# Kernel tuning notes

Hardware: AMD Instinct MI355X
Metric: run time of the kernel (lower is better)

The kernel has to match this reference:

```python
import jax, jax.numpy as jnp
import numpy as np
import math

B, T = 64, 2000
RNN_DIM, EMB_DIM, ATT_DIM = 1024, 512, 128
STATIC_CH, STATIC_K = 8, 21
DYN_CH, DYN_K = 8, 21
PRIOR_LEN, ALPHA, BETA = 11, 0.1, 0.9


def _betabinom_pmf(k, n, a, b):
    lg = math.lgamma
    return math.exp(lg(n + 1) - lg(k + 1) - lg(n - k + 1)
                    + lg(k + a) + lg(n - k + b) - lg(n + a + b)
                    - (lg(a) + lg(b) - lg(a + b)))


def setup_inputs() -> dict:
    key = jax.random.key(0)
    ks = jax.random.split(key, 12)
    query = jax.random.normal(ks[0], (B, RNN_DIM), jnp.float32)
    memory = jax.random.normal(ks[1], (B, T, EMB_DIM), jnp.float32)
    a = jax.random.uniform(ks[2], (B, T), jnp.float32)
    alignment_pre = a / jnp.sum(a, axis=1, keepdims=True)  # valid attention distribution
    mask = jnp.zeros((B, T), dtype=bool)
    s = 1.0 / math.sqrt(RNN_DIM)
    W_w = jax.random.uniform(ks[3], (ATT_DIM, RNN_DIM), jnp.float32, -s, s)
    W_b = jax.random.uniform(ks[4], (ATT_DIM,), jnp.float32, -s, s)
    V_w = jax.random.normal(ks[5], (DYN_CH * DYN_K, ATT_DIM), jnp.float32) * 0.05
    F_w = jax.random.normal(ks[6], (STATIC_CH, 1, STATIC_K), jnp.float32) * 0.1
    U_w = jax.random.normal(ks[7], (ATT_DIM, STATIC_CH), jnp.float32) * 0.1
    T_w = jax.random.normal(ks[8], (ATT_DIM, DYN_CH), jnp.float32) * 0.1
    T_b = jax.random.normal(ks[9], (ATT_DIM,), jnp.float32) * 0.05
    v_w = jax.random.normal(ks[10], (1, ATT_DIM), jnp.float32) * 0.1
    P_np = np.array([_betabinom_pmf(k, PRIOR_LEN - 1, ALPHA, BETA) for k in range(PRIOR_LEN)], np.float32)
    P = jnp.asarray(P_np[::-1].copy())  # buffer: flipped beta-binomial prior
    return {"attention_hidden_state": query, "memory": memory, "alignment_pre": alignment_pre,
            "mask": mask, "W_w": W_w, "W_b": W_b, "V_w": V_w, "F_w": F_w,
            "U_w": U_w, "T_w": T_w, "T_b": T_b, "v_w": v_w, "P": P}


def _conv1d(lhs, rhs, pad, groups=1):
    # lhs [N,C,T], rhs [O,C//groups,K]; cross-correlation, matching torch conv1d
    return jax.lax.conv_general_dilated(lhs, rhs, (1,), [pad],
                                        dimension_numbers=("NCH", "OIH", "NCH"),
                                        feature_group_count=groups)


def reference(attention_hidden_state, memory, alignment_pre, mask,
              W_w, W_b, V_w, F_w, U_w, T_w, T_b, v_w, P):
    b, t = alignment_pre.shape
    # log of causal beta-binomial prior: left-pad by prior_length-1, valid conv
    p = _conv1d(alignment_pre[:, None, :], P.reshape(1, 1, -1), (PRIOR_LEN - 1, 0))[:, 0, :]
    p = jnp.log(jnp.clip(p, 1e-6))
    # per-sample dynamic kernels: [B, dyn_ch*K]
    G = jnp.tanh(attention_hidden_state @ W_w.T + W_b) @ V_w.T
    g = _conv1d(alignment_pre[None, :, :], G.reshape(b * DYN_CH, 1, DYN_K),
                ((DYN_K - 1) // 2, (DYN_K - 1) // 2), groups=b)  # [1, B*dyn_ch, T]
    g = g.reshape(b, DYN_CH, t).transpose(0, 2, 1)  # [B, T, dyn_ch]
    # static conv features
    f = _conv1d(alignment_pre[:, None, :], F_w,
                ((STATIC_K - 1) // 2, (STATIC_K - 1) // 2)).transpose(0, 2, 1)  # [B, T, static_ch]
    e = (jnp.tanh(f @ U_w.T + g @ T_w.T + T_b) @ v_w.T)[..., 0] + p  # [B, T]
    e = jnp.where(mask, -jnp.inf, e)
    attention_weights = jax.nn.softmax(e, axis=1)
    attention_context = jnp.einsum("bt,bte->be", attention_weights, memory)
    return attention_context, attention_weights
```

## Files before the change

### kernel.cpp

```cpp
#include <hip/hip_runtime.h>

#define B_   64
#define T_   2000
#define RNN_ 1024
#define EMB_ 512
#define ATT_ 128
#define CH_  8
#define K_   21
#define PL_  11
#define GSZ  168
#define ECHK 128
#define NEC  16
#define CCHK 40
#define NCC  50

typedef float vf4 __attribute__((ext_vector_type(4)));

__device__ __forceinline__ float fast_tanh(float x) {
    float ax = fabsf(x);
    float e  = __expf(2.0f * ax);
    float t  = 1.0f - 2.0f / (e + 1.0f);
    return copysignf(t, x);
}

__global__ __launch_bounds__(256) void k_gen_dyn(
    const float* __restrict__ q, const float* __restrict__ Ww,
    const float* __restrict__ Wb, const float* __restrict__ Vw,
    float* __restrict__ G, float* __restrict__ out_ctx)
{
    __shared__ float sq[RNN_];
    __shared__ float part[256];
    __shared__ float sh[ATT_];
    const int b = blockIdx.x, tid = threadIdx.x;
    for (int i = tid; i < EMB_; i += 256) out_ctx[b * EMB_ + i] = 0.f;
    for (int i = tid; i < RNN_; i += 256) sq[i] = q[b * RNN_ + i];
    __syncthreads();
    {
        const int row = tid & 127, half = tid >> 7;
        const float4* wr = reinterpret_cast<const float4*>(Ww + row * RNN_ + half * (RNN_ / 2));
        const float4* qr = reinterpret_cast<const float4*>(sq + half * (RNN_ / 2));
        float acc = 0.f;
        #pragma unroll 8
        for (int i = 0; i < RNN_ / 8; ++i) {
            float4 w4 = wr[i], q4 = qr[i];
            acc += w4.x * q4.x + w4.y * q4.y + w4.z * q4.z + w4.w * q4.w;
        }
        part[tid] = acc;
    }
    __syncthreads();
    if (tid < ATT_) sh[tid] = fast_tanh(part[tid] + part[tid + 128] + Wb[tid]);
    __syncthreads();
    for (int o = tid; o < GSZ; o += 256) {
        const float4* vr = reinterpret_cast<const float4*>(Vw + o * ATT_);
        const float4* hr = reinterpret_cast<const float4*>(sh);
        float acc = 0.f;
        #pragma unroll 8
        for (int i = 0; i < ATT_ / 4; ++i) {
            float4 v4 = vr[i], h4 = hr[i];
            acc += v4.x * h4.x + v4.y * h4.y + v4.z * h4.z + v4.w * h4.w;
        }
        G[b * GSZ + o] = acc;
    }
}

__global__ __launch_bounds__(256) void k_energy(
    const float* __restrict__ a,  const float* __restrict__ G,
    const float* __restrict__ Fw, const float* __restrict__ Uw,
    const float* __restrict__ Tw, const float* __restrict__ Tb,
    const float* __restrict__ vw, const float* __restrict__ P,
    const unsigned char* __restrict__ mask,
    float* __restrict__ pws, float* __restrict__ sred)
{
    __shared__ float sA[ECHK + K_ - 1];
    __shared__ float sFG[K_ * 16];
    __shared__ float sUT[ATT_ * 16];
    __shared__ float sTb[ATT_], sV[ATT_], sPr[PL_];
    __shared__ float sQ[2 * ECHK];
    __shared__ float red[4];
    const int b = blockIdx.x, chunk = blockIdx.y, tid = threadIdx.x;
    const int t0 = chunk * ECHK;
    const int tloc = tid & (ECHK - 1);
    const int h = tid >> 7;

    for (int j = tid; j < ECHK + K_ - 1; j += 256) {
        int idx = t0 - 10 + j;
        sA[j] = (idx >= 0 && idx < T_) ? a[b * T_ + idx] : 0.f;
    }
    for (int j = tid; j < 2 * GSZ; j += 256) {
        if (j < GSZ) sFG[(j % K_) * 16 + (j / K_)] = Fw[j];
        else { int jj = j - GSZ; sFG[(jj % K_) * 16 + 8 + (jj / K_)] = G[b * GSZ + jj]; }
    }
    for (int j = tid; j < ATT_ * CH_; j += 256) {
        int d = j >> 3, c = j & 7;
        sUT[d * 16 + c]     = Uw[j];
        sUT[d * 16 + 8 + c] = Tw[j];
    }
    if (tid < ATT_) { sTb[tid] = Tb[tid]; sV[tid] = vw[tid]; }
    if (tid < PL_)  sPr[tid] = P[tid];
    __syncthreads();

    float fg[16];
    #pragma unroll
    for (int i = 0; i < 16; ++i) fg[i] = 0.f;
    #pragma unroll
    for (int k = 0; k < K_; ++k) {
        float av = sA[tloc + k];
        const float4* fp = reinterpret_cast<const float4*>(&sFG[k * 16]);
        float4 x0 = fp[0], x1 = fp[1], x2 = fp[2], x3 = fp[3];
        fg[0]  += x0.x * av; fg[1]  += x0.y * av; fg[2]  += x0.z * av; fg[3]  += x0.w * av;
        fg[4]  += x1.x * av; fg[5]  += x1.y * av; fg[6]  += x1.z * av; fg[7]  += x1.w * av;
        fg[8]  += x2.x * av; fg[9]  += x2.y * av; fg[10] += x2.z * av; fg[11] += x2.w * av;
        fg[12] += x3.x * av; fg[13] += x3.y * av; fg[14] += x3.z * av; fg[15] += x3.w * av;
    }

    float accQ = 0.f;
    const int d0 = h * 64;
    #pragma unroll 4
    for (int dd = 0; dd < 64; ++dd) {
        const int d = d0 + dd;
        const float4* up = reinterpret_cast<const float4*>(&sUT[d * 16]);
        float4 u0 = up[0], u1 = up[1], u2 = up[2], u3 = up[3];
        float s0 = u0.x * fg[0]  + u0.y * fg[1]  + u0.z * fg[2]  + u0.w * fg[3];
        float s1 = u1.x * fg[4]  + u1.y * fg[5]  + u1.z * fg[6]  + u1.w * fg[7];
        float s2 = u2.x * fg[8]  + u2.y * fg[9]  + u2.z * fg[10] + u2.w * fg[11];
        float s3 = u3.x * fg[12] + u3.y * fg[13] + u3.z * fg[14] + u3.w * fg[15];
        float s = (sTb[d] + s0) + (s1 + s2) + s3;
        accQ += sV[d] * fast_tanh(s);
    }
    sQ[h * ECHK + tloc] = accQ;
    __syncthreads();

    float pv = 0.f;
    const int t = t0 + tid;
    if (tid < ECHK) {
        if (!mask[b * T_ + min(t, T_ - 1)] && t < T_) {
            float pp = 0.f;
            #pragma unroll
            for (int k = 0; k < PL_; ++k) pp += sPr[k] * sA[tid + k];
            float e = sQ[tid] + sQ[ECHK + tid] + __logf(fmaxf(pp, 1e-6f));
            pv = __expf(e);
        }
        if (t < T_) pws[b * T_ + t] = pv;
    }
    float ssum = pv;
    #pragma unroll
    for (int off = 32; off > 0; off >>= 1) ssum += __shfl_xor(ssum, off);
    if ((tid & 63) == 0) red[tid >> 6] = ssum;
    __syncthreads();
    if (tid == 0) sred[b * NEC + chunk] = red[0] + red[1] + red[2] + red[3];
}

__global__ __launch_bounds__(256, 4) void k_ctx(
    const float* __restrict__ sred, const float* __restrict__ pws,
    const float* __restrict__ mem, float* __restrict__ wout,
    float* __restrict__ out)
{
    __shared__ float sw_[CCHK];
    __shared__ vf4 sCtx[2][EMB_ / 4];
    const int b = blockIdx.x, chunk = blockIdx.y, tid = threadIdx.x;
    const int t0 = chunk * CCHK;
    const int col = tid & 127, rp = tid >> 7;
    const float* basep = mem + ((size_t)(b * T_ + t0)) * EMB_ + col * 4;

    const float4* sp = reinterpret_cast<const float4*>(sred + b * NEC);
    float4 s0 = sp[0], s1 = sp[1], s2 = sp[2], s3 = sp[3];
    float S = ((s0.x + s0.y) + (s0.z + s0.w)) + ((s1.x + s1.y) + (s1.z + s1.w))
            + ((s2.x + s2.y) + (s2.z + s2.w)) + ((s3.x + s3.y) + (s3.z + s3.w));
    const float inv = 1.0f / S;

    if (tid < CCHK) {
        float wv = pws[b * T_ + t0 + tid] * inv;
        sw_[tid] = wv;
        wout[b * T_ + t0 + tid] = wv;
    }
    __syncthreads();

    vf4 acc0 = {0.f, 0.f, 0.f, 0.f}, acc1 = {0.f, 0.f, 0.f, 0.f};
    #pragma unroll
    for (int i = 0; i < CCHK / 4; ++i) {
        const int r0 = rp + i * 4;
        const int r1 = rp + i * 4 + 2;
        vf4 m0 = *reinterpret_cast<const vf4*>(basep + (size_t)r0 * EMB_);
        vf4 m1 = *reinterpret_cast<const vf4*>(basep + (size_t)r1 * EMB_);
        acc0 += sw_[r0] * m0;
        acc1 += sw_[r1] * m1;
    }
    sCtx[rp][col] = acc0 + acc1;
    __syncthreads();
    if (tid < 128) {
        vf4 r = sCtx[0][tid];
        r += sCtx[1][tid];
        float* op = out + b * EMB_ + tid * 4;
        atomicAdd(op + 0, r.x); atomicAdd(op + 1, r.y);
        atomicAdd(op + 2, r.z); atomicAdd(op + 3, r.w);
    }
}

extern "C" void kernel_launch(void* const* d_in, const int* in_sizes, int n_in,
                              void* d_out, int out_size, void* d_ws, size_t ws_size,
                              hipStream_t stream)
{
    const float* q    = (const float*)d_in[0];
    const float* mem  = (const float*)d_in[1];
    const float* a    = (const float*)d_in[2];
    const unsigned char* mask = (const unsigned char*)d_in[3];
    const float* Ww = (const float*)d_in[4];
    const float* Wb = (const float*)d_in[5];
    const float* Vw = (const float*)d_in[6];
    const float* Fw = (const float*)d_in[7];
    const float* Uw = (const float*)d_in[8];
    const float* Tw = (const float*)d_in[9];
    const float* Tb = (const float*)d_in[10];
    const float* vw = (const float*)d_in[11];
    const float* P  = (const float*)d_in[12];

    float* out_ctx = (float*)d_out;
    float* out_w   = out_ctx + B_ * EMB_;

    float* G    = (float*)d_ws;
    float* sred = G + B_ * GSZ;
    float* pws  = sred + B_ * NEC;

    k_gen_dyn<<<B_, 256, 0, stream>>>(q, Ww, Wb, Vw, G, out_ctx);
    k_energy<<<dim3(B_, NEC), 256, 0, stream>>>(a, G, Fw, Uw, Tw, Tb, vw, P,
                                                mask, pws, sred);
    k_ctx<<<dim3(B_, NCC), 256, 0, stream>>>(sred, pws, mem, out_w, out_ctx);
}
```

Measured before the change: 101.0 us.

## Read energy weights straight from global memory and widen context chunks

The energy kernel no longer stages the filter, projection, bias and prior weights in shared memory. It reads them directly from global memory, which drops the staging loops and one source of LDS traffic but depends on those uniform loads being cached. The context kernel now uses 64-row chunks (32 chunks per batch), with a tail path for the last partial chunk and a higher occupancy hint in launch bounds. This gives fewer blocks and atomics per batch but adds a branch and may underfill the GPU.

```diff
diff --git a/kernel.cpp b/kernel.cpp
--- a/kernel.cpp
+++ b/kernel.cpp
@@ -11,8 +11,8 @@
 #define GSZ  168
 #define ECHK 128
 #define NEC  16
-#define CCHK 40
-#define NCC  50
+#define CCHK 64
+#define NCC  32
 
 typedef float vf4 __attribute__((ext_vector_type(4)));
 
@@ -72,9 +72,6 @@
     float* __restrict__ pws, float* __restrict__ sred)
 {
     __shared__ float sA[ECHK + K_ - 1];
-    __shared__ float sFG[K_ * 16];
-    __shared__ float sUT[ATT_ * 16];
-    __shared__ float sTb[ATT_], sV[ATT_], sPr[PL_];
     __shared__ float sQ[2 * ECHK];
     __shared__ float red[4];
     const int b = blockIdx.x, chunk = blockIdx.y, tid = threadIdx.x;
@@ -86,31 +83,20 @@
         int idx = t0 - 10 + j;
         sA[j] = (idx >= 0 && idx < T_) ? a[b * T_ + idx] : 0.f;
     }
-    for (int j = tid; j < 2 * GSZ; j += 256) {
-        if (j < GSZ) sFG[(j % K_) * 16 + (j / K_)] = Fw[j];
-        else { int jj = j - GSZ; sFG[(jj % K_) * 16 + 8 + (jj / K_)] = G[b * GSZ + jj]; }
-    }
-    for (int j = tid; j < ATT_ * CH_; j += 256) {
-        int d = j >> 3, c = j & 7;
-        sUT[d * 16 + c]     = Uw[j];
-        sUT[d * 16 + 8 + c] = Tw[j];
-    }
-    if (tid < ATT_) { sTb[tid] = Tb[tid]; sV[tid] = vw[tid]; }
-    if (tid < PL_)  sPr[tid] = P[tid];
-    __syncthreads();
-
+    __syncthreads();
+
+    const float* __restrict__ Gb = G + b * GSZ;
     float fg[16];
     #pragma unroll
     for (int i = 0; i < 16; ++i) fg[i] = 0.f;
     #pragma unroll
     for (int k = 0; k < K_; ++k) {
         float av = sA[tloc + k];
-        const float4* fp = reinterpret_cast<const float4*>(&sFG[k * 16]);
-        float4 x0 = fp[0], x1 = fp[1], x2 = fp[2], x3 = fp[3];
-        fg[0]  += x0.x * av; fg[1]  += x0.y * av; fg[2]  += x0.z * av; fg[3]  += x0.w * av;
-        fg[4]  += x1.x * av; fg[5]  += x1.y * av; fg[6]  += x1.z * av; fg[7]  += x1.w * av;
-        fg[8]  += x2.x * av; fg[9]  += x2.y * av; fg[10] += x2.z * av; fg[11] += x2.w * av;
-        fg[12] += x3.x * av; fg[13] += x3.y * av; fg[14] += x3.z * av; fg[15] += x3.w * av;
+        #pragma unroll
+        for (int c = 0; c < CH_; ++c) {
+            fg[c]     += Fw[c * K_ + k] * av;
+            fg[8 + c] += Gb[c * K_ + k] * av;
+        }
     }
 
     float accQ = 0.f;
@@ -118,14 +104,12 @@
     #pragma unroll 4
     for (int dd = 0; dd < 64; ++dd) {
         const int d = d0 + dd;
-        const float4* up = reinterpret_cast<const float4*>(&sUT[d * 16]);
-        float4 u0 = up[0], u1 = up[1], u2 = up[2], u3 = up[3];
-        float s0 = u0.x * fg[0]  + u0.y * fg[1]  + u0.z * fg[2]  + u0.w * fg[3];
-        float s1 = u1.x * fg[4]  + u1.y * fg[5]  + u1.z * fg[6]  + u1.w * fg[7];
-        float s2 = u2.x * fg[8]  + u2.y * fg[9]  + u2.z * fg[10] + u2.w * fg[11];
-        float s3 = u3.x * fg[12] + u3.y * fg[13] + u3.z * fg[14] + u3.w * fg[15];
-        float s = (sTb[d] + s0) + (s1 + s2) + s3;
-        accQ += sV[d] * fast_tanh(s);
+        const float* __restrict__ u = Uw + d * CH_;
+        const float* __restrict__ tw = Tw + d * CH_;
+        float s = Tb[d];
+        #pragma unroll
+        for (int c = 0; c < CH_; ++c) s += u[c] * fg[c] + tw[c] * fg[8 + c];
+        accQ += vw[d] * fast_tanh(s);
     }
     sQ[h * ECHK + tloc] = accQ;
     __syncthreads();
@@ -133,10 +117,10 @@
     float pv = 0.f;
     const int t = t0 + tid;
     if (tid < ECHK) {
-        if (!mask[b * T_ + min(t, T_ - 1)] && t < T_) {
+        if (t < T_ && !mask[b * T_ + min(t, T_ - 1)]) {
             float pp = 0.f;
             #pragma unroll
-            for (int k = 0; k < PL_; ++k) pp += sPr[k] * sA[tid + k];
+            for (int k = 0; k < PL_; ++k) pp += P[k] * sA[tid + k];
             float e = sQ[tid] + sQ[ECHK + tid] + __logf(fmaxf(pp, 1e-6f));
             pv = __expf(e);
         }
@@ -150,7 +134,7 @@
     if (tid == 0) sred[b * NEC + chunk] = red[0] + red[1] + red[2] + red[3];
 }
 
-__global__ __launch_bounds__(256, 4) void k_ctx(
+__global__ __launch_bounds__(256, 8) void k_ctx(
     const float* __restrict__ sred, const float* __restrict__ pws,
     const float* __restrict__ mem, float* __restrict__ wout,
     float* __restrict__ out)
@@ -159,8 +143,8 @@
     __shared__ vf4 sCtx[2][EMB_ / 4];
     const int b = blockIdx.x, chunk = blockIdx.y, tid = threadIdx.x;
     const int t0 = chunk * CCHK;
+    const int nvalid = min(CCHK, T_ - t0);
     const int col = tid & 127, rp = tid >> 7;
-    const float* basep = mem + ((size_t)(b * T_ + t0)) * EMB_ + col * 4;
 
     const float4* sp = reinterpret_cast<const float4*>(sred + b * NEC);
     float4 s0 = sp[0], s1 = sp[1], s2 = sp[2], s3 = sp[3];
@@ -169,21 +153,32 @@
     const float inv = 1.0f / S;
 
     if (tid < CCHK) {
-        float wv = pws[b * T_ + t0 + tid] * inv;
+        const int t = t0 + tid;
+        float wv = 0.f;
+        if (t < T_) {
+            wv = pws[b * T_ + t] * inv;
+            wout[b * T_ + t] = wv;
+        }
         sw_[tid] = wv;
-        wout[b * T_ + t0 + tid] = wv;
-    }
-    __syncthreads();
-
+    }
+    __syncthreads();
+
+    const float* basep = mem + ((size_t)(b * T_ + t0)) * EMB_ + col * 4;
     vf4 acc0 = {0.f, 0.f, 0.f, 0.f}, acc1 = {0.f, 0.f, 0.f, 0.f};
-    #pragma unroll
-    for (int i = 0; i < CCHK / 4; ++i) {
-        const int r0 = rp + i * 4;
-        const int r1 = rp + i * 4 + 2;
-        vf4 m0 = *reinterpret_cast<const vf4*>(basep + (size_t)r0 * EMB_);
-        vf4 m1 = *reinterpret_cast<const vf4*>(basep + (size_t)r1 * EMB_);
-        acc0 += sw_[r0] * m0;
-        acc1 += sw_[r1] * m1;
+    if (nvalid == CCHK) {
+        #pragma unroll
+        for (int i = 0; i < CCHK / 4; ++i) {
+            const int r0 = rp + 4 * i, r1 = rp + 4 * i + 2;
+            vf4 m0 = *reinterpret_cast<const vf4*>(basep + (size_t)r0 * EMB_);
+            vf4 m1 = *reinterpret_cast<const vf4*>(basep + (size_t)r1 * EMB_);
+            acc0 += sw_[r0] * m0;
+            acc1 += sw_[r1] * m1;
+        }
+    } else {
+        for (int tt = rp; tt < nvalid; tt += 2) {
+            vf4 mv = *reinterpret_cast<const vf4*>(basep + (size_t)tt * EMB_);
+            acc0 += sw_[tt] * mv;
+        }
     }
     sCtx[rp][col] = acc0 + acc1;
     __syncthreads();
```

Result: slower. 107.0 us (+6.0%).
